# Kernel optimization log

Hardware: AMD Instinct MI355X
Metric: run time of the kernel (lower is better)

The kernel has to match this reference:

```python
import jax, jax.numpy as jnp
import numpy as np

N = 100000      # nodes
E = 1600000     # edges
IN_F = 128
CL1 = 64
CL2 = 64
OUT_F = 2
G = 128         # graphs in batch


def setup_inputs() -> dict:
    key = jax.random.key(0)
    ks = jax.random.split(key, 9)
    x = jax.random.normal(ks[0], (N, IN_F), dtype=jnp.float32)
    edge_index = jax.random.randint(ks[1], (2, E), 0, N, dtype=jnp.int64)
    batch = jnp.sort(jax.random.randint(ks[2], (N,), 0, G, dtype=jnp.int64))
    # Glorot-ish init for GCN weights, PyG Linear-style for the head
    W1 = jax.random.normal(ks[3], (IN_F, CL1), dtype=jnp.float32) / np.sqrt(IN_F)
    b1 = jnp.zeros((CL1,), dtype=jnp.float32)
    W2 = jax.random.normal(ks[4], (CL1, CL2), dtype=jnp.float32) / np.sqrt(CL1)
    b2 = jnp.zeros((CL2,), dtype=jnp.float32)
    Wlin = jax.random.normal(ks[5], (CL2 * 3, OUT_F), dtype=jnp.float32) / np.sqrt(CL2 * 3)
    blin = jnp.zeros((OUT_F,), dtype=jnp.float32)
    return dict(x=x, W1=W1, b1=b1, W2=W2, b2=b2, Wlin=Wlin, blin=blin,
                edge_index=edge_index, batch=batch, num_graphs=G)


def gcn_conv(x, src, dst, W, b):
    """PyG GCNConv: add self-loops, symmetric normalization, x@W, scatter-add, +bias."""
    n = x.shape[0]
    xw = x @ W  # [N, out_c] -- transform BEFORE propagate (PyG order)
    loop = jnp.arange(n, dtype=src.dtype)
    s = jnp.concatenate([src, loop])  # sources incl. self loops
    d = jnp.concatenate([dst, loop])  # destinations incl. self loops
    deg = jax.ops.segment_sum(jnp.ones(s.shape, x.dtype), d, num_segments=n)
    dinv = jnp.where(deg > 0, jax.lax.rsqrt(deg), 0.0)
    norm = dinv[s] * dinv[d]                      # [E+N]
    msg = xw[s] * norm[:, None]                   # gather + scale
    return jax.ops.segment_sum(msg, d, num_segments=n) + b


def reference(x, W1, b1, W2, b2, Wlin, blin, edge_index, batch, num_graphs):
    src, dst = edge_index[0], edge_index[1]
    h = jax.nn.relu(gcn_conv(x, src, dst, W1, b1))
    h = jax.nn.relu(gcn_conv(h, src, dst, W2, b2))
    # global add / mean / max pooling over graphs
    x0 = jax.ops.segment_sum(h, batch, num_segments=num_graphs)
    cnt = jax.ops.segment_sum(jnp.ones((h.shape[0],), h.dtype), batch, num_segments=num_graphs)
    x1 = x0 / jnp.maximum(cnt, 1.0)[:, None]
    x2 = jax.ops.segment_max(h, batch, num_segments=num_graphs)
    x2 = jnp.where(jnp.isfinite(x2), x2, 0.0)  # empty segments -> 0
    xcat = jnp.concatenate([x0, x1, x2], axis=-1)  # [G, 3*CL2]
    out = xcat @ Wlin + blin                       # [G, OUT_F]
    return (xcat, out)
```

## Files before the change

kernel.cpp:

```cpp
#include <hip/hip_runtime.h>

#define IN_F 128
#define C1 64
#define NG 128
#define CAT 192
#define DCAP 10240

typedef unsigned short u16;
typedef unsigned int u32;
typedef __attribute__((ext_vector_type(8))) short bf16x8;
typedef __attribute__((ext_vector_type(4))) float f32x4;

__device__ inline u16 f2bf(float f) {
  u32 u = __float_as_uint(f);
  u = (u + 0x7FFFu + ((u >> 16) & 1u)) >> 16;
  return (u16)u;
}
__device__ inline float bf2f(u16 h) { return __uint_as_float(((u32)h) << 16); }
__device__ inline float bflo(u32 p) { return __uint_as_float(p << 16); }
__device__ inline float bfhi(u32 p) { return __uint_as_float(p & 0xFFFF0000u); }


__global__ void zero_k(int* __restrict__ g, int n) {
  int i = blockIdx.x * 256 + threadIdx.x;
  if (i < n) g[i] = 0;
}


__global__ __launch_bounds__(256) void stage_k(const int* __restrict__ src,
                                               const int* __restrict__ dst, int e,
                                               int* __restrict__ gcur,
                                               u32* __restrict__ stage, int ndig) {
  __shared__ int h4[4][256];
  __shared__ int h[256];
  __shared__ int cur[256];
  int t = threadIdx.x;
  int wv = t >> 6;
  h4[0][t] = 0; h4[1][t] = 0; h4[2][t] = 0; h4[3][t] = 0;
  __syncthreads();
  int base = blockIdx.x * 4096;
  int mys[16], myd[16];
  #pragma unroll
  for (int i = 0; i < 16; i++) {
    int j = base + t + i * 256;
    if (j < e) {
      mys[i] = src[j];
      myd[i] = dst[j];
      atomicAdd(&h4[wv][myd[i] >> 9], 1);
    } else {
      myd[i] = -1;
    }
  }
  __syncthreads();
  int cnt = h4[0][t] + h4[1][t] + h4[2][t] + h4[3][t];
  int gbase = 0;
  if (t < ndig && cnt > 0) gbase = atomicAdd(&gcur[t], cnt);
  h[t] = gbase;
  cur[t] = 0;
  __syncthreads();
  #pragma unroll
  for (int i = 0; i < 16; i++) {
    if (myd[i] >= 0) {
      int d = myd[i] >> 9;
      int r = atomicAdd(&cur[d], 1);
      stage[(size_t)d * DCAP + h[d] + r] = (u32)mys[i] | ((u32)(myd[i] & 511) << 17);
    }
  }
}

__global__ __launch_bounds__(256) void csr_k(const u32* __restrict__ stage,
                                             const int* __restrict__ gcur,
                                             int* __restrict__ rowptr,
                                             int* __restrict__ counts,
                                             float* __restrict__ dinv,
                                             int* __restrict__ csr, int n) {
  __shared__ int hc[512];
  __shared__ int hb[512];
  __shared__ int cu[512];
  __shared__ int sc[256];
  int dg = blockIdx.x;
  int t = threadIdx.x;
  int n0 = dg * 512;
  int nloc = min(n - n0, 512);
  int e0 = dg * DCAP;
  int e1 = e0 + gcur[dg];
  hc[t] = 0; hc[t + 256] = 0;
  __syncthreads();
  for (int j = e0 + t; j < e1; j += 256) atomicAdd(&hc[stage[j] >> 17], 1);
  __syncthreads();
  int a0 = hc[2 * t], a1 = hc[2 * t + 1];
  int s = a0 + a1;
  sc[t] = s;
  __syncthreads();
  #pragma unroll
  for (int off = 1; off < 256; off <<= 1) {
    int x = sc[t] + ((t >= off) ? sc[t - off] : 0);
    __syncthreads();
    sc[t] = x;
    __syncthreads();
  }
  int excl = sc[t] - s;
  hb[2 * t] = excl;
  hb[2 * t + 1] = excl + a0;
  cu[2 * t] = 0; cu[2 * t + 1] = 0;
  __syncthreads();
  for (int i = t; i < nloc; i += 256) {
    int node = n0 + i;
    rowptr[node] = e0 + hb[i];
    counts[node] = hc[i];
    dinv[node] = rsqrtf((float)hc[i] + 1.0f);
  }
  __syncthreads();
  for (int j = e0 + t; j < e1; j += 256) {
    u32 p = stage[j];
    int li = p >> 17;
    int r = atomicAdd(&cu[li], 1);
    csr[e0 + hb[li] + r] = (int)(p & 0x1FFFFu);
  }
}


template <int K, bool IN_BF16>
__global__ __launch_bounds__(256) void gemm_mfma_k(const void* __restrict__ Xv,
                                                   const float* __restrict__ W,
                                                   u16* __restrict__ Y, int n) {
  constexpr int KK = K / 32;
  constexpr int XSN = 2048 * KK;
  constexpr int TOT = 4096 * KK;
  constexpr int SMEMN = (TOT > 9216) ? TOT : 9216;
  __shared__ u16 smem[SMEMN];
  u16* Xs = smem;
  u16* Ws = smem + XSN;
  int t = threadIdx.x;
  int row0 = blockIdx.x * 64;

  for (int idx = t; idx < K * 16; idx += 256) {
    int k = idx >> 4, c4 = (idx & 15) * 4;
    float4 wv = *(const float4*)(W + (size_t)k * 64 + c4);
    int kk = k >> 5, k8 = (k & 31) >> 3, kr = k & 7;
    float wa[4] = {wv.x, wv.y, wv.z, wv.w};
    #pragma unroll
    for (int j = 0; j < 4; j++) {
      int c = c4 + j;
      u32 byte = (u32)(((kk * 64 + c) * 32 + k8 * 8 + kr) * 2);
      byte ^= (u32)((c & 7) << 4);
      *(u16*)((char*)Ws + byte) = f2bf(wa[j]);
    }
  }

  for (int idx = t; idx < 8 * K; idx += 256) {
    int r = idx / (K / 8);
    int c8 = idx % (K / 8);
    int gr = row0 + r;
    u16 vals[8];
    if (gr < n) {
      if (IN_BF16) {
        *(uint4*)vals = *(const uint4*)((const u16*)Xv + (size_t)gr * K + c8 * 8);
      } else {
        const float4 x0 = *(const float4*)((const float*)Xv + (size_t)gr * K + c8 * 8);
        const float4 x1 = *(const float4*)((const float*)Xv + (size_t)gr * K + c8 * 8 + 4);
        vals[0] = f2bf(x0.x); vals[1] = f2bf(x0.y); vals[2] = f2bf(x0.z); vals[3] = f2bf(x0.w);
        vals[4] = f2bf(x1.x); vals[5] = f2bf(x1.y); vals[6] = f2bf(x1.z); vals[7] = f2bf(x1.w);
      }
    } else {
      #pragma unroll
      for (int j = 0; j < 8; j++) vals[j] = 0;
    }
    int wrow = r >> 4, row = r & 15, kk = c8 >> 2, k8 = c8 & 3;
    u32 byte = (u32)((((wrow * KK + kk) * 16 + row) * 32 + k8 * 8) * 2);
    byte ^= (u32)((row & 7) << 4);
    *(uint4*)((char*)Xs + byte) = *(uint4*)vals;
  }
  __syncthreads();

  int w = t >> 6, l = t & 63;
  int lrow = l & 15, lk = l >> 4;
  bf16x8 bfrag[KK][4];
  #pragma unroll
  for (int kk = 0; kk < KK; kk++) {
    #pragma unroll
    for (int cb = 0; cb < 4; cb++) {
      int col = cb * 16 + lrow;
      u32 byte = (u32)(((kk * 64 + col) * 32 + lk * 8) * 2);
      byte ^= (u32)((col & 7) << 4);
      bfrag[kk][cb] = *(bf16x8*)((char*)Ws + byte);
    }
  }
  f32x4 acc[4] = {};
  #pragma unroll
  for (int kk = 0; kk < KK; kk++) {
    u32 abyte = (u32)((((w * KK + kk) * 16 + lrow) * 32 + lk * 8) * 2);
    abyte ^= (u32)((lrow & 7) << 4);
    bf16x8 a = *(bf16x8*)((char*)Xs + abyte);
    #pragma unroll
    for (int cb = 0; cb < 4; cb++) {
      acc[cb] = __builtin_amdgcn_mfma_f32_16x16x32_bf16(a, bfrag[kk][cb], acc[cb], 0, 0, 0);
    }
  }
  __syncthreads();

  #pragma unroll
  for (int cb = 0; cb < 4; cb++) {
    #pragma unroll
    for (int reg = 0; reg < 4; reg++) {
      int r = w * 16 + lk * 4 + reg;
      int c = cb * 16 + lrow;
      smem[r * 72 + c] = f2bf(acc[cb][reg]);
    }
  }
  __syncthreads();
  #pragma unroll
  for (int p = 0; p < 2; p++) {
    int idx = t + p * 256;
    int rr = idx >> 3, ch = idx & 7;
    int gr = row0 + rr;
    if (gr < n) {
      uint4 v = *(uint4*)&smem[rr * 72 + ch * 8];
      *(uint4*)(Y + (size_t)gr * 64 + ch * 8) = v;
    }
  }
}


__device__ __forceinline__ void gather_node(const u16* __restrict__ xw,
                                            const int* __restrict__ rowptr,
                                            const int* __restrict__ counts,
                                            const int* __restrict__ csr,
                                            const float* __restrict__ dinv,
                                            const float* __restrict__ bias,
                                            int nid, int lane, float acc[8]) {
  float di = dinv[nid];
  float sc = di * di;
  {
    uint4 a = *(const uint4*)(xw + (size_t)nid * 64 + lane * 8);
    acc[0] = bflo(a.x) * sc; acc[1] = bfhi(a.x) * sc;
    acc[2] = bflo(a.y) * sc; acc[3] = bfhi(a.y) * sc;
    acc[4] = bflo(a.z) * sc; acc[5] = bfhi(a.z) * sc;
    acc[6] = bflo(a.w) * sc; acc[7] = bfhi(a.w) * sc;
  }
  int st = rowptr[nid];
  int cn = counts[nid];
  int myidx = 0;
  float dv = 0.f;
  if (lane < cn) {
    myidx = csr[st + lane];
    dv = dinv[myidx];
  }
  for (int c = 0; c < cn; c += 8) {
    int rem = cn - c;
    uint4 vv[8];
    #pragma unroll
    for (int i = 0; i < 8; i++) {
      int s = __shfl(myidx, i, 8);
      if (i < rem) {
        vv[i] = *(const uint4*)(xw + (size_t)s * 64 + lane * 8);
      } else {
        vv[i] = make_uint4(0, 0, 0, 0);
      }
    }
    float ww[8];
    float myw = dv * di;
    #pragma unroll
    for (int i = 0; i < 8; i++) ww[i] = (i < rem) ? __shfl(myw, i, 8) : 0.f;
    int nxt = 0;
    float ndv = 0.f;
    if (c + 8 < cn && lane < rem - 8) {
      nxt = csr[st + c + 8 + lane];
      ndv = dinv[nxt];
    }
    #pragma unroll
    for (int i = 0; i < 8; i++) {
      float wgt = ww[i];
      acc[0] += bflo(vv[i].x) * wgt; acc[1] += bfhi(vv[i].x) * wgt;
      acc[2] += bflo(vv[i].y) * wgt; acc[3] += bfhi(vv[i].y) * wgt;
      acc[4] += bflo(vv[i].z) * wgt; acc[5] += bfhi(vv[i].z) * wgt;
      acc[6] += bflo(vv[i].w) * wgt; acc[7] += bfhi(vv[i].w) * wgt;
    }
    myidx = nxt;
    dv = ndv;
  }
  const float4 b0 = *(const float4*)(bias + lane * 8);
  const float4 b1 = *(const float4*)(bias + lane * 8 + 4);
  acc[0] = fmaxf(acc[0] + b0.x, 0.f);
  acc[1] = fmaxf(acc[1] + b0.y, 0.f);
  acc[2] = fmaxf(acc[2] + b0.z, 0.f);
  acc[3] = fmaxf(acc[3] + b0.w, 0.f);
  acc[4] = fmaxf(acc[4] + b1.x, 0.f);
  acc[5] = fmaxf(acc[5] + b1.y, 0.f);
  acc[6] = fmaxf(acc[6] + b1.z, 0.f);
  acc[7] = fmaxf(acc[7] + b1.w, 0.f);
}

__global__ __launch_bounds__(256) void gather_k(const u16* __restrict__ xw,
                                                u16* __restrict__ hout,
                                                const int* __restrict__ rowptr,
                                                const int* __restrict__ counts,
                                                const int* __restrict__ csr,
                                                const float* __restrict__ dinv,
                                                const float* __restrict__ bias, int n) {
  int idx = blockIdx.x * 256 + threadIdx.x;
  int nid = idx >> 3;
  int lane = idx & 7;
  if (nid >= n) return;
  float acc[8];
  gather_node(xw, rowptr, counts, csr, dinv, bias, nid, lane, acc);
  uint4 o;
  o.x = ((u32)f2bf(acc[0])) | ((u32)f2bf(acc[1]) << 16);
  o.y = ((u32)f2bf(acc[2])) | ((u32)f2bf(acc[3]) << 16);
  o.z = ((u32)f2bf(acc[4])) | ((u32)f2bf(acc[5]) << 16);
  o.w = ((u32)f2bf(acc[6])) | ((u32)f2bf(acc[7]) << 16);
  *(uint4*)(hout + (size_t)nid * 64 + lane * 8) = o;
}

__global__ __launch_bounds__(256) void gpool_k(const u16* __restrict__ xw,
                                               const int* __restrict__ rowptr,
                                               const int* __restrict__ counts,
                                               const int* __restrict__ csr,
                                               const float* __restrict__ dinv,
                                               const float* __restrict__ bias,
                                               const int* __restrict__ batch,
                                               float* __restrict__ gsum,
                                               u32* __restrict__ gmax, int n) {
  __shared__ float rows[32][68];
  __shared__ int rowg[32];
  int t = threadIdx.x;
  int idx = blockIdx.x * 256 + t;
  int nid = idx >> 3;
  int lane = idx & 7;
  int nl = t >> 3;
  bool active = nid < n;
  float acc[8] = {0.f, 0.f, 0.f, 0.f, 0.f, 0.f, 0.f, 0.f};
  int g = -1;
  if (active) {
    gather_node(xw, rowptr, counts, csr, dinv, bias, nid, lane, acc);
    g = batch[nid];
  }
  if (lane == 0) rowg[nl] = g;
  *(float4*)&rows[nl][lane * 8]     = make_float4(acc[0], acc[1], acc[2], acc[3]);
  *(float4*)&rows[nl][lane * 8 + 4] = make_float4(acc[4], acc[5], acc[6], acc[7]);
  int gfirst0 = batch[(blockIdx.x * 256) >> 3];
  if (active && g - gfirst0 >= 4) {
    #pragma unroll
    for (int i = 0; i < 8; i++) {
      atomicAdd(&gsum[g * 64 + lane * 8 + i], acc[i]);
      atomicMax(&gmax[g * 64 + lane * 8 + i], __float_as_uint(acc[i]));
    }
    if (lane == 0) rowg[nl] = -1;
  }
  __syncthreads();
  int gfirst = rowg[0];
  int gl = t >> 6;
  int f = t & 63;
  int gg = gfirst + gl;
  float s = 0.f, m = 0.f;
  bool any = false;
  #pragma unroll 8
  for (int r = 0; r < 32; r++) {
    if (rowg[r] == gg) {
      float v = rows[r][f];
      s += v;
      m = fmaxf(m, v);
      any = true;
    }
  }
  if (any && gg >= 0 && gg < NG) {
    atomicAdd(&gsum[gg * 64 + f], s);
    atomicMax(&gmax[gg * 64 + f], __float_as_uint(m));
  }
}


__global__ __launch_bounds__(64) void fin_k(const float* __restrict__ gsum,
                                            const u32* __restrict__ gmax,
                                            const int* __restrict__ batch, int n,
                                            const float* __restrict__ Wlin,
                                            const float* __restrict__ blin,
                                            float* __restrict__ xcat,
                                            float* __restrict__ outh) {
  int g = blockIdx.x;
  int lane = threadIdx.x;
  __shared__ int se[2];
  if (lane < 2) {
    int target = g + lane;
    int lo = 0, hi = n;
    while (lo < hi) {
      int mid = (lo + hi) >> 1;
      if (batch[mid] < target) lo = mid + 1; else hi = mid;
    }
    se[lane] = lo;
  }
  __syncthreads();
  int cnt = se[1] - se[0];
  float x0 = gsum[g * 64 + lane];
  float x1 = x0 / fmaxf((float)cnt, 1.0f);
  float x2 = __uint_as_float(gmax[g * 64 + lane]);
  xcat[g * CAT + lane]       = x0;
  xcat[g * CAT + 64 + lane]  = x1;
  xcat[g * CAT + 128 + lane] = x2;
  #pragma unroll
  for (int o = 0; o < 2; o++) {
    float p = x0 * Wlin[lane * 2 + o] +
              x1 * Wlin[(64 + lane) * 2 + o] +
              x2 * Wlin[(128 + lane) * 2 + o];
    #pragma unroll
    for (int off = 32; off > 0; off >>= 1) p += __shfl_down(p, off, 64);
    if (lane == 0) outh[g * 2 + o] = p + blin[o];
  }
}


extern "C" void kernel_launch(void* const* d_in, const int* in_sizes, int n_in,
                              void* d_out, int out_size, void* d_ws, size_t ws_size,
                              hipStream_t stream) {
  const float* x    = (const float*)d_in[0];
  const float* W1   = (const float*)d_in[1];
  const float* b1   = (const float*)d_in[2];
  const float* W2   = (const float*)d_in[3];
  const float* b2   = (const float*)d_in[4];
  const float* Wlin = (const float*)d_in[5];
  const float* blin = (const float*)d_in[6];
  const int*   ei   = (const int*)d_in[7];
  const int*   batch= (const int*)d_in[8];

  const int N = in_sizes[0] / IN_F;
  const int E = in_sizes[7] / 2;
  const int* src = ei;
  const int* dst = ei + E;
  const int ndig = (N + 511) >> 9;
  const int nbE  = (E + 4095) / 4096;

  char* w = (char*)d_ws;
  auto alloc = [&](size_t bytes) {
    void* p = (void*)w;
    w += (bytes + 255) & ~(size_t)255;
    return p;
  };
  int*   rowptr = (int*)alloc((size_t)N * 4);
  int*   counts = (int*)alloc((size_t)N * 4);
  float* dinv   = (float*)alloc((size_t)N * 4);
  int*   csr    = (int*)alloc((size_t)ndig * DCAP * 4);
  int*   zbuf   = (int*)alloc((size_t)(256 + 2 * NG * 64) * 4);
  u16*   bufA   = (u16*)alloc((size_t)N * 64 * 2);
  u16*   bufB   = (u16*)alloc((size_t)N * 64 * 2);
  u32*   stage  = (u32*)alloc((size_t)ndig * DCAP * 4);

  int*   gcur = zbuf;
  float* gsum = (float*)(zbuf + 256);
  u32*   gmax = (u32*)(zbuf + 256 + NG * 64);

  float* xcat = (float*)d_out;
  float* outh = (float*)d_out + NG * CAT;

  const int nz = 256 + 2 * NG * 64;
  zero_k  <<<(nz + 255) / 256, 256, 0, stream>>>(zbuf, nz);
  stage_k <<<nbE, 256, 0, stream>>>(src, dst, E, gcur, stage, ndig);
  csr_k   <<<ndig, 256, 0, stream>>>(stage, gcur, rowptr, counts, dinv, csr, N);

  gemm_mfma_k<IN_F, false> <<<(N + 63) / 64, 256, 0, stream>>>(x, W1, bufA, N);
  gather_k <<<(N * 8 + 255) / 256, 256, 0, stream>>>(bufA, bufB, rowptr, counts, csr, dinv, b1, N);

  gemm_mfma_k<C1, true> <<<(N + 63) / 64, 256, 0, stream>>>(bufB, W2, bufA, N);
  gpool_k <<<(N * 8 + 255) / 256, 256, 0, stream>>>(bufA, rowptr, counts, csr, dinv, b2,
                                                    batch, gsum, gmax, N);

  fin_k <<<NG, 64, 0, stream>>>(gsum, gmax, batch, N, Wlin, blin, xcat, outh);
}
```

Before: 159.2 us.

## Coalesce staging and CSR writes via LDS, fold zeroing, widen pooling blocks

stage_k now sorts each block's edges by destination bucket in LDS using a prefix scan, then writes them to the staging buffer in contiguous runs instead of scattered per-edge stores. csr_k builds each bucket's CSR in a 40KB LDS buffer and writes it out linearly, and it also zeroes the pooling accumulators, so zero_k shrinks to clearing only gcur. gpool_k handles 128 nodes per block instead of 32, which cuts the number of global atomic reductions per graph. The costs are more LDS per block, which may lower occupancy, and extra scan barriers.

```diff
diff --git a/kernel.cpp b/kernel.cpp
--- a/kernel.cpp
+++ b/kernel.cpp
@@ -7,6 +7,7 @@
 #define DCAP 10240
 
 typedef unsigned short u16;
+typedef unsigned char u8;
 typedef unsigned int u32;
 typedef __attribute__((ext_vector_type(8))) short bf16x8;
 typedef __attribute__((ext_vector_type(4))) float f32x4;
@@ -21,10 +22,7 @@
 __device__ inline float bfhi(u32 p) { return __uint_as_float(p & 0xFFFF0000u); }
 
 
-__global__ void zero_k(int* __restrict__ g, int n) {
-  int i = blockIdx.x * 256 + threadIdx.x;
-  if (i < n) g[i] = 0;
-}
+__global__ void zero_k(int* __restrict__ g) { g[threadIdx.x] = 0; }
 
 
 __global__ __launch_bounds__(256) void stage_k(const int* __restrict__ src,
@@ -32,13 +30,17 @@
                                                int* __restrict__ gcur,
                                                u32* __restrict__ stage, int ndig) {
   __shared__ int h4[4][256];
-  __shared__ int h[256];
-  __shared__ int cur[256];
+  __shared__ int sc[256];
+  __shared__ int lcur[256];
+  __shared__ int loff[256];
+  __shared__ u32 ebuf[4096];
+  __shared__ u8  dbuf[4096];
   int t = threadIdx.x;
   int wv = t >> 6;
   h4[0][t] = 0; h4[1][t] = 0; h4[2][t] = 0; h4[3][t] = 0;
   __syncthreads();
   int base = blockIdx.x * 4096;
+  int tot = min(4096, e - base);
   int mys[16], myd[16];
   #pragma unroll
   for (int i = 0; i < 16; i++) {
@@ -53,18 +55,34 @@
   }
   __syncthreads();
   int cnt = h4[0][t] + h4[1][t] + h4[2][t] + h4[3][t];
+  sc[t] = cnt;
+  __syncthreads();
+  #pragma unroll
+  for (int off = 1; off < 256; off <<= 1) {
+    int x = sc[t] + ((t >= off) ? sc[t - off] : 0);
+    __syncthreads();
+    sc[t] = x;
+    __syncthreads();
+  }
+  int excl = sc[t] - cnt;
   int gbase = 0;
   if (t < ndig && cnt > 0) gbase = atomicAdd(&gcur[t], cnt);
-  h[t] = gbase;
-  cur[t] = 0;
+  lcur[t] = excl;
+  loff[t] = t * DCAP + gbase - excl;
   __syncthreads();
   #pragma unroll
   for (int i = 0; i < 16; i++) {
     if (myd[i] >= 0) {
       int d = myd[i] >> 9;
-      int r = atomicAdd(&cur[d], 1);
-      stage[(size_t)d * DCAP + h[d] + r] = (u32)mys[i] | ((u32)(myd[i] & 511) << 17);
-    }
+      int r = atomicAdd(&lcur[d], 1);
+      ebuf[r] = (u32)mys[i] | ((u32)(myd[i] & 511) << 17);
+      dbuf[r] = (u8)d;
+    }
+  }
+  __syncthreads();
+  for (int j = t; j < tot; j += 256) {
+    int d = dbuf[j];
+    stage[loff[d] + j] = ebuf[j];
   }
 }
 
@@ -73,20 +91,26 @@
                                              int* __restrict__ rowptr,
                                              int* __restrict__ counts,
                                              float* __restrict__ dinv,
-                                             int* __restrict__ csr, int n) {
+                                             int* __restrict__ csr,
+                                             int* __restrict__ zeroA, int nz, int n) {
   __shared__ int hc[512];
   __shared__ int hb[512];
   __shared__ int cu[512];
   __shared__ int sc[256];
+  __shared__ u32 lbuf[DCAP];
   int dg = blockIdx.x;
   int t = threadIdx.x;
+  {
+    int zi = dg * 256 + t;
+    if (zi < nz) zeroA[zi] = 0;
+  }
   int n0 = dg * 512;
   int nloc = min(n - n0, 512);
   int e0 = dg * DCAP;
-  int e1 = e0 + gcur[dg];
+  int cntE = gcur[dg];
   hc[t] = 0; hc[t + 256] = 0;
   __syncthreads();
-  for (int j = e0 + t; j < e1; j += 256) atomicAdd(&hc[stage[j] >> 17], 1);
+  for (int j = t; j < cntE; j += 256) atomicAdd(&hc[stage[e0 + j] >> 17], 1);
   __syncthreads();
   int a0 = hc[2 * t], a1 = hc[2 * t + 1];
   int s = a0 + a1;
@@ -111,12 +135,14 @@
     dinv[node] = rsqrtf((float)hc[i] + 1.0f);
   }
   __syncthreads();
-  for (int j = e0 + t; j < e1; j += 256) {
-    u32 p = stage[j];
+  for (int j = t; j < cntE; j += 256) {
+    u32 p = stage[e0 + j];
     int li = p >> 17;
     int r = atomicAdd(&cu[li], 1);
-    csr[e0 + hb[li] + r] = (int)(p & 0x1FFFFu);
-  }
+    lbuf[hb[li] + r] = p & 0x1FFFFu;
+  }
+  __syncthreads();
+  for (int j = t; j < cntE; j += 256) csr[e0 + j] = (int)lbuf[j];
 }
 
 
@@ -321,41 +347,42 @@
                                                const int* __restrict__ batch,
                                                float* __restrict__ gsum,
                                                u32* __restrict__ gmax, int n) {
-  __shared__ float rows[32][68];
-  __shared__ int rowg[32];
+  __shared__ float rows[128][68];
+  __shared__ int rowg[128];
   int t = threadIdx.x;
-  int idx = blockIdx.x * 256 + t;
-  int nid = idx >> 3;
-  int lane = idx & 7;
-  int nl = t >> 3;
-  bool active = nid < n;
-  float acc[8] = {0.f, 0.f, 0.f, 0.f, 0.f, 0.f, 0.f, 0.f};
-  int g = -1;
-  if (active) {
-    gather_node(xw, rowptr, counts, csr, dinv, bias, nid, lane, acc);
-    g = batch[nid];
-  }
-  if (lane == 0) rowg[nl] = g;
-  *(float4*)&rows[nl][lane * 8]     = make_float4(acc[0], acc[1], acc[2], acc[3]);
-  *(float4*)&rows[nl][lane * 8 + 4] = make_float4(acc[4], acc[5], acc[6], acc[7]);
-  int gfirst0 = batch[(blockIdx.x * 256) >> 3];
-  if (active && g - gfirst0 >= 4) {
-    #pragma unroll
-    for (int i = 0; i < 8; i++) {
-      atomicAdd(&gsum[g * 64 + lane * 8 + i], acc[i]);
-      atomicMax(&gmax[g * 64 + lane * 8 + i], __float_as_uint(acc[i]));
-    }
-    if (lane == 0) rowg[nl] = -1;
-  }
-  __syncthreads();
-  int gfirst = rowg[0];
+  int grp = t >> 3;
+  int lane = t & 7;
+  int nbase = blockIdx.x * 128;
+  int gfirst = batch[nbase < n ? nbase : (n - 1)];
+  for (int p = 0; p < 4; p++) {
+    int nl = p * 32 + grp;
+    int nid = nbase + nl;
+    float acc[8] = {0.f, 0.f, 0.f, 0.f, 0.f, 0.f, 0.f, 0.f};
+    int g = -1;
+    if (nid < n) {
+      gather_node(xw, rowptr, counts, csr, dinv, bias, nid, lane, acc);
+      g = batch[nid];
+      if (g - gfirst >= 4) {
+        #pragma unroll
+        for (int i = 0; i < 8; i++) {
+          atomicAdd(&gsum[g * 64 + lane * 8 + i], acc[i]);
+          atomicMax(&gmax[g * 64 + lane * 8 + i], __float_as_uint(acc[i]));
+        }
+        g = -1;
+      }
+    }
+    if (lane == 0) rowg[nl] = g;
+    *(float4*)&rows[nl][lane * 8]     = make_float4(acc[0], acc[1], acc[2], acc[3]);
+    *(float4*)&rows[nl][lane * 8 + 4] = make_float4(acc[4], acc[5], acc[6], acc[7]);
+  }
+  __syncthreads();
   int gl = t >> 6;
   int f = t & 63;
   int gg = gfirst + gl;
   float s = 0.f, m = 0.f;
   bool any = false;
   #pragma unroll 8
-  for (int r = 0; r < 32; r++) {
+  for (int r = 0; r < 128; r++) {
     if (rowg[r] == gg) {
       float v = rows[r][f];
       s += v;
@@ -363,7 +390,7 @@
       any = true;
     }
   }
-  if (any && gg >= 0 && gg < NG) {
+  if (any && gg < NG) {
     atomicAdd(&gsum[gg * 64 + f], s);
     atomicMax(&gmax[gg * 64 + f], __float_as_uint(m));
   }
@@ -451,17 +478,17 @@
   float* xcat = (float*)d_out;
   float* outh = (float*)d_out + NG * CAT;
 
-  const int nz = 256 + 2 * NG * 64;
-  zero_k  <<<(nz + 255) / 256, 256, 0, stream>>>(zbuf, nz);
+  zero_k  <<<1, 256, 0, stream>>>(gcur);
   stage_k <<<nbE, 256, 0, stream>>>(src, dst, E, gcur, stage, ndig);
-  csr_k   <<<ndig, 256, 0, stream>>>(stage, gcur, rowptr, counts, dinv, csr, N);
+  csr_k   <<<ndig, 256, 0, stream>>>(stage, gcur, rowptr, counts, dinv, csr,
+                                     zbuf + 256, 2 * NG * 64, N);
 
   gemm_mfma_k<IN_F, false> <<<(N + 63) / 64, 256, 0, stream>>>(x, W1, bufA, N);
   gather_k <<<(N * 8 + 255) / 256, 256, 0, stream>>>(bufA, bufB, rowptr, counts, csr, dinv, b1, N);
 
   gemm_mfma_k<C1, true> <<<(N + 63) / 64, 256, 0, stream>>>(bufB, W2, bufA, N);
-  gpool_k <<<(N * 8 + 255) / 256, 256, 0, stream>>>(bufA, rowptr, counts, csr, dinv, b2,
-                                                    batch, gsum, gmax, N);
+  gpool_k <<<(N + 127) / 128, 256, 0, stream>>>(bufA, rowptr, counts, csr, dinv, b2,
+                                                batch, gsum, gmax, N);
 
   fin_k <<<NG, 64, 0, stream>>>(gsum, gmax, batch, N, Wlin, blin, xcat, outh);
 }
```

Result: no change. 156.1 us (-1.9%).
